# Performance work log

Measured on AMD Instinct MI355X. Metric: run time of the kernel, lower is better.

Reference implementation:

```python
import jax, jax.numpy as jnp
import numpy as np

IN_FEATURES = 4096
OUT_FEATURES = 11008
NUM_GROUPS = 4


def setup_inputs() -> dict:
    key = jax.random.key(0)
    k1, k2, k3 = jax.random.split(key, 3)
    inp = jax.random.normal(k1, (16, IN_FEATURES), dtype=jnp.float32)
    # packed int2 weights: each byte holds 4 ternary values (stored biased by +1 in 2 bits)
    weight_packed = jax.random.randint(k2, (OUT_FEATURES, IN_FEATURES // 4), 0, 256, dtype=jnp.int32)
    weight_scale = jax.random.uniform(k3, (NUM_GROUPS,), dtype=jnp.float32, minval=0.5, maxval=1.5)
    return {"input": inp, "weight_packed": weight_packed, "weight_scale": weight_scale}


def _unpack_int2(weight_packed):
    # [M, K/4] packed bytes -> [M, K] ternary values in {-1, 0, 1, 2}
    p = weight_packed
    M, Kp = p.shape
    w = jnp.stack([p & 3, (p >> 2) & 3, (p >> 4) & 3, (p >> 6) & 3], axis=-1)
    return w.reshape(M, Kp * 4).astype(jnp.float32) - 1.0


def reference(input, weight_packed, weight_scale):
    # per-row int8 activation quantization
    s = 127.0 / jnp.clip(jnp.max(jnp.abs(input), axis=-1, keepdims=True), 1e-5)  # [B,1]
    q = jnp.clip(jnp.round(input * s), -128.0, 127.0)  # int8-valued floats [B,K]
    w = _unpack_int2(weight_packed)  # [M,K]
    out = q @ w.T  # [B,M] integer-valued accumulation
    M = weight_packed.shape[0]
    rows_per_group = M // weight_scale.shape[0]
    col_scale = jnp.repeat(weight_scale, rows_per_group)  # [M] per-output-group scale
    return out * (1.0 / s) * col_scale
```

## Files before the change

### kernel.cpp

```cpp
#include <hip/hip_runtime.h>
#include <stdint.h>

#define K_DIM 4096
#define KW 1024
#define M_DIM 11008
#define B_DIM 16
#define GROUP_ROWS 2752
#define QTR_W 256

typedef int v4i __attribute__((ext_vector_type(4)));

__device__ __forceinline__ int spread2(int p) {
    int t = p | (p << 12);
    return (t & 0x00030003) | (((t >> 2) & 0x00030003) << 8);
}

__global__ __launch_bounds__(1024) void quant_k(const float* __restrict__ in,
                                                int* __restrict__ qg,
                                                int* __restrict__ sumq,
                                                float* __restrict__ invs) {
    const int b = blockIdx.x, t = threadIdx.x;
    const int lane = t & 63, wid = t >> 6;

    float4 v = ((const float4*)(in + (size_t)b * K_DIM))[t];
    float mx = fmaxf(fmaxf(fabsf(v.x), fabsf(v.y)), fmaxf(fabsf(v.z), fabsf(v.w)));
#pragma unroll
    for (int s = 1; s < 64; s <<= 1) mx = fmaxf(mx, __shfl_xor(mx, s, 64));

    __shared__ float wmax[16];
    __shared__ int wsum[16];
    if (lane == 0) wmax[wid] = mx;
    __syncthreads();
    float bm = wmax[0];
#pragma unroll
    for (int i = 1; i < 16; ++i) bm = fmaxf(bm, wmax[i]);
    const float sc = 127.f / fmaxf(bm, 1e-5f);

    float xs[4] = {v.x, v.y, v.z, v.w};
    int w = 0, ss = 0;
#pragma unroll
    for (int j = 0; j < 4; ++j) {
        int q = (int)rintf(xs[j] * sc);
        q = q > 127 ? 127 : (q < -128 ? -128 : q);
        ss += q;
        w |= (q & 255) << (8 * j);
    }
    qg[b * KW + t] = w;

#pragma unroll
    for (int s = 1; s < 64; s <<= 1) ss += __shfl_xor(ss, s, 64);
    if (lane == 0) wsum[wid] = ss;
    __syncthreads();
    if (t == 0) {
        int tot = 0;
#pragma unroll
        for (int i = 0; i < 16; ++i) tot += wsum[i];
        sumq[b] = tot;
        invs[b] = fmaxf(bm, 1e-5f) / 127.f;
    }
}

__global__ __launch_bounds__(256) void gemm_k(const int* __restrict__ wp,
                                              const int* __restrict__ qg,
                                              const int* __restrict__ sumq,
                                              const float* __restrict__ invs,
                                              const float* __restrict__ wscale,
                                              float* __restrict__ out) {
    __shared__ v4i buf[2][1024];
    const int t = threadIdx.x, lane = t & 63, wid = t >> 6;
    const int m0 = blockIdx.x * 16;
    const int lrow = lane & 15;
    const int lgrp = lane >> 4;

    const int* qbase = qg + lrow * KW + wid * 64 + lgrp * 4;

    v4i acc = {0, 0, 0, 0};
    v4i wst[4];
    v4i qb[2][4];

#pragma unroll
    for (int r = 0; r < 4; ++r) {
        const int row = r * 4 + wid;
        wst[r] = *(const v4i*)(wp + (size_t)(m0 + row) * KW + lane * 4);
    }
#pragma unroll
    for (int s = 0; s < 4; ++s) qb[0][s] = *(const v4i*)(qbase + s * 16);
#pragma unroll
    for (int r = 0; r < 4; ++r) {
        const int row = r * 4 + wid;
        buf[0][row * 64 + (lane ^ (row & 7))] = wst[r];
    }
    asm volatile("s_waitcnt lgkmcnt(0)" ::: "memory");
    asm volatile("s_barrier" ::: "memory");

#pragma unroll
    for (int q = 0; q < 4; ++q) {
        if (q < 3) {
#pragma unroll
            for (int r = 0; r < 4; ++r) {
                const int row = r * 4 + wid;
                wst[r] = *(const v4i*)(wp + (size_t)(m0 + row) * KW + (q + 1) * QTR_W + lane * 4);
            }
#pragma unroll
            for (int s = 0; s < 4; ++s)
                qb[(q + 1) & 1][s] = *(const v4i*)(qbase + (q + 1) * QTR_W + s * 16);
        }
#pragma unroll
        for (int s = 0; s < 4; ++s) {
            const int c = wid * 16 + s * 4 + lgrp;
            v4i wv = buf[q & 1][lrow * 64 + (c ^ (lrow & 7))];
            v4i bb;
            bb[0] = spread2(wv[0]); bb[1] = spread2(wv[1]);
            bb[2] = spread2(wv[2]); bb[3] = spread2(wv[3]);
            acc = __builtin_amdgcn_mfma_i32_16x16x64_i8(qb[q & 1][s], bb, acc, 0, 0, 0);
        }
        asm volatile("s_barrier" ::: "memory");
        if (q < 3) {
#pragma unroll
            for (int r = 0; r < 4; ++r) {
                const int row = r * 4 + wid;
                buf[(q + 1) & 1][row * 64 + (lane ^ (row & 7))] = wst[r];
            }
            asm volatile("s_waitcnt lgkmcnt(0)" ::: "memory");
            asm volatile("s_barrier" ::: "memory");
        }
    }

    buf[0][wid * 64 + lane] = acc;
    asm volatile("s_waitcnt lgkmcnt(0)" ::: "memory");
    asm volatile("s_barrier" ::: "memory");

    const int b = t >> 4, m = t & 15;
    const int src_lane = ((b >> 2) << 4) | m;
    const int reg = b & 3;
    const int* red = (const int*)&buf[0][0];
    int sum = red[(0 * 64 + src_lane) * 4 + reg] + red[(1 * 64 + src_lane) * 4 + reg] +
              red[(2 * 64 + src_lane) * 4 + reg] + red[(3 * 64 + src_lane) * 4 + reg];
    const float val = (float)(sum - sumq[b]) * invs[b] * wscale[m0 / GROUP_ROWS];
    out[(size_t)b * M_DIM + m0 + m] = val;
}

extern "C" void kernel_launch(void* const* d_in, const int* in_sizes, int n_in,
                              void* d_out, int out_size, void* d_ws, size_t ws_size,
                              hipStream_t stream) {
    const float* inp    = (const float*)d_in[0];
    const int*   wp     = (const int*)d_in[1];
    const float* wscale = (const float*)d_in[2];
    float* out = (float*)d_out;

    int*   qg   = (int*)d_ws;
    int*   sumq = qg + B_DIM * KW;
    float* invs = (float*)(sumq + B_DIM);

    quant_k<<<dim3(B_DIM), dim3(1024), 0, stream>>>(inp, qg, sumq, invs);
    gemm_k<<<dim3(M_DIM / 16), dim3(256), 0, stream>>>(wp, qg, sumq, invs, wscale, out);
}
```

Measured before the change: 21.24 us.

## Stream weights via direct global-to-LDS loads with triple buffering and split quant kernel

The GEMM kernel now loads packed weights straight into LDS with global_load_lds into a three-stage ring buffer, prefetching two quarters ahead and synchronising with vmcnt waits. This replaces the old register staging and extra LDS write barriers. All quantized activations are preloaded into registers up front. The quant kernel is split into 64 blocks of 256 threads, each redoing the row max, and writes partial sums that the GEMM adds up. The cost is more register pressure and redundant max computation.

Result: slower. 30.35 us (+42.9%).

```diff
diff --git a/kernel.cpp b/kernel.cpp
--- a/kernel.cpp
+++ b/kernel.cpp
@@ -15,28 +15,42 @@
     return (t & 0x00030003) | (((t >> 2) & 0x00030003) << 8);
 }
 
-__global__ __launch_bounds__(1024) void quant_k(const float* __restrict__ in,
-                                                int* __restrict__ qg,
-                                                int* __restrict__ sumq,
-                                                float* __restrict__ invs) {
-    const int b = blockIdx.x, t = threadIdx.x;
-    const int lane = t & 63, wid = t >> 6;
+__device__ __forceinline__ void gload_lds16(const int* g, int* l) {
+    __builtin_amdgcn_global_load_lds(
+        (const __attribute__((address_space(1))) unsigned int*)g,
+        (__attribute__((address_space(3))) unsigned int*)l, 16, 0, 0);
+}
 
-    float4 v = ((const float4*)(in + (size_t)b * K_DIM))[t];
-    float mx = fmaxf(fmaxf(fabsf(v.x), fabsf(v.y)), fmaxf(fabsf(v.z), fabsf(v.w)));
+__global__ __launch_bounds__(256) void quant_k(const float* __restrict__ in,
+                                               int* __restrict__ qg,
+                                               int* __restrict__ sumq_part,
+                                               float* __restrict__ invs) {
+    const int g = blockIdx.x, b = g >> 2, qt = g & 3;
+    const int t = threadIdx.x, lane = t & 63, wid = t >> 6;
+
+    const float4* row = (const float4*)(in + (size_t)b * K_DIM);
+    float4 v[4];
+#pragma unroll
+    for (int i = 0; i < 4; ++i) v[i] = row[t + i * 256];
+
+    float mx = 0.f;
+#pragma unroll
+    for (int i = 0; i < 4; ++i) {
+        mx = fmaxf(mx, fabsf(v[i].x)); mx = fmaxf(mx, fabsf(v[i].y));
+        mx = fmaxf(mx, fabsf(v[i].z)); mx = fmaxf(mx, fabsf(v[i].w));
+    }
 #pragma unroll
     for (int s = 1; s < 64; s <<= 1) mx = fmaxf(mx, __shfl_xor(mx, s, 64));
 
-    __shared__ float wmax[16];
-    __shared__ int wsum[16];
+    __shared__ float wmax[4];
+    __shared__ int wsum[4];
     if (lane == 0) wmax[wid] = mx;
     __syncthreads();
-    float bm = wmax[0];
-#pragma unroll
-    for (int i = 1; i < 16; ++i) bm = fmaxf(bm, wmax[i]);
+    const float bm = fmaxf(fmaxf(wmax[0], wmax[1]), fmaxf(wmax[2], wmax[3]));
     const float sc = 127.f / fmaxf(bm, 1e-5f);
 
-    float xs[4] = {v.x, v.y, v.z, v.w};
+    const float4 mine = v[qt];
+    float xs[4] = {mine.x, mine.y, mine.z, mine.w};
     int w = 0, ss = 0;
 #pragma unroll
     for (int j = 0; j < 4; ++j) {
@@ -45,98 +59,86 @@
         ss += q;
         w |= (q & 255) << (8 * j);
     }
-    qg[b * KW + t] = w;
+    qg[b * KW + qt * QTR_W + t] = w;
 
 #pragma unroll
     for (int s = 1; s < 64; s <<= 1) ss += __shfl_xor(ss, s, 64);
     if (lane == 0) wsum[wid] = ss;
     __syncthreads();
     if (t == 0) {
-        int tot = 0;
-#pragma unroll
-        for (int i = 0; i < 16; ++i) tot += wsum[i];
-        sumq[b] = tot;
-        invs[b] = fmaxf(bm, 1e-5f) / 127.f;
+        sumq_part[b * 4 + qt] = wsum[0] + wsum[1] + wsum[2] + wsum[3];
+        if (qt == 0) invs[b] = fmaxf(bm, 1e-5f) / 127.f;
     }
 }
 
-__global__ __launch_bounds__(256) void gemm_k(const int* __restrict__ wp,
-                                              const int* __restrict__ qg,
-                                              const int* __restrict__ sumq,
-                                              const float* __restrict__ invs,
-                                              const float* __restrict__ wscale,
-                                              float* __restrict__ out) {
-    __shared__ v4i buf[2][1024];
+__global__ __launch_bounds__(256, 4) void gemm_k(const int* __restrict__ wp,
+                                                 const int* __restrict__ qg,
+                                                 const int* __restrict__ sumq_part,
+                                                 const float* __restrict__ invs,
+                                                 const float* __restrict__ wscale,
+                                                 float* __restrict__ out) {
+    __shared__ v4i bufv[3 * 1024];
+    int* bufi = (int*)bufv;
     const int t = threadIdx.x, lane = t & 63, wid = t >> 6;
     const int m0 = blockIdx.x * 16;
     const int lrow = lane & 15;
     const int lgrp = lane >> 4;
 
-    const int* qbase = qg + lrow * KW + wid * 64 + lgrp * 4;
+    v4i qr[16];
+#pragma unroll
+    for (int i = 0; i < 16; ++i) {
+        const int qq = i >> 2, s = i & 3;
+        qr[i] = *(const v4i*)(qg + lrow * KW + qq * QTR_W + wid * 64 + s * 16 + lgrp * 4);
+    }
+#pragma unroll
+    for (int qq = 0; qq < 2; ++qq) {
+#pragma unroll
+        for (int r = 0; r < 4; ++r) {
+            const int row = r * 4 + wid;
+            gload_lds16(wp + (size_t)(m0 + row) * KW + qq * QTR_W + (lane ^ (row & 7)) * 4,
+                        bufi + qq * 4096 + row * 256);
+        }
+    }
 
     v4i acc = {0, 0, 0, 0};
-    v4i wst[4];
-    v4i qb[2][4];
-
-#pragma unroll
-    for (int r = 0; r < 4; ++r) {
-        const int row = r * 4 + wid;
-        wst[r] = *(const v4i*)(wp + (size_t)(m0 + row) * KW + lane * 4);
-    }
-#pragma unroll
-    for (int s = 0; s < 4; ++s) qb[0][s] = *(const v4i*)(qbase + s * 16);
-#pragma unroll
-    for (int r = 0; r < 4; ++r) {
-        const int row = r * 4 + wid;
-        buf[0][row * 64 + (lane ^ (row & 7))] = wst[r];
-    }
-    asm volatile("s_waitcnt lgkmcnt(0)" ::: "memory");
-    asm volatile("s_barrier" ::: "memory");
 
 #pragma unroll
     for (int q = 0; q < 4; ++q) {
-        if (q < 3) {
+        if (q < 3) asm volatile("s_waitcnt vmcnt(4)" ::: "memory");
+        else       asm volatile("s_waitcnt vmcnt(0)" ::: "memory");
+        asm volatile("s_barrier" ::: "memory");
+        if (q < 2) {
+            const int nb = (q + 2) % 3;
 #pragma unroll
             for (int r = 0; r < 4; ++r) {
                 const int row = r * 4 + wid;
-                wst[r] = *(const v4i*)(wp + (size_t)(m0 + row) * KW + (q + 1) * QTR_W + lane * 4);
+                gload_lds16(wp + (size_t)(m0 + row) * KW + (q + 2) * QTR_W + (lane ^ (row & 7)) * 4,
+                            bufi + nb * 4096 + row * 256);
             }
-#pragma unroll
-            for (int s = 0; s < 4; ++s)
-                qb[(q + 1) & 1][s] = *(const v4i*)(qbase + (q + 1) * QTR_W + s * 16);
         }
 #pragma unroll
         for (int s = 0; s < 4; ++s) {
             const int c = wid * 16 + s * 4 + lgrp;
-            v4i wv = buf[q & 1][lrow * 64 + (c ^ (lrow & 7))];
+            v4i wv = bufv[(q % 3) * 1024 + lrow * 64 + (c ^ (lrow & 7))];
             v4i bb;
             bb[0] = spread2(wv[0]); bb[1] = spread2(wv[1]);
             bb[2] = spread2(wv[2]); bb[3] = spread2(wv[3]);
-            acc = __builtin_amdgcn_mfma_i32_16x16x64_i8(qb[q & 1][s], bb, acc, 0, 0, 0);
-        }
-        asm volatile("s_barrier" ::: "memory");
-        if (q < 3) {
-#pragma unroll
-            for (int r = 0; r < 4; ++r) {
-                const int row = r * 4 + wid;
-                buf[(q + 1) & 1][row * 64 + (lane ^ (row & 7))] = wst[r];
-            }
-            asm volatile("s_waitcnt lgkmcnt(0)" ::: "memory");
-            asm volatile("s_barrier" ::: "memory");
+            acc = __builtin_amdgcn_mfma_i32_16x16x64_i8(qr[q * 4 + s], bb, acc, 0, 0, 0);
         }
     }
 
-    buf[0][wid * 64 + lane] = acc;
-    asm volatile("s_waitcnt lgkmcnt(0)" ::: "memory");
-    asm volatile("s_barrier" ::: "memory");
+    __syncthreads();
+    bufv[wid * 64 + lane] = acc;
+    __syncthreads();
 
     const int b = t >> 4, m = t & 15;
     const int src_lane = ((b >> 2) << 4) | m;
     const int reg = b & 3;
-    const int* red = (const int*)&buf[0][0];
-    int sum = red[(0 * 64 + src_lane) * 4 + reg] + red[(1 * 64 + src_lane) * 4 + reg] +
-              red[(2 * 64 + src_lane) * 4 + reg] + red[(3 * 64 + src_lane) * 4 + reg];
-    const float val = (float)(sum - sumq[b]) * invs[b] * wscale[m0 / GROUP_ROWS];
+    int sum = bufi[(0 * 64 + src_lane) * 4 + reg] + bufi[(1 * 64 + src_lane) * 4 + reg] +
+              bufi[(2 * 64 + src_lane) * 4 + reg] + bufi[(3 * 64 + src_lane) * 4 + reg];
+    const int sq = sumq_part[b * 4 + 0] + sumq_part[b * 4 + 1] +
+                   sumq_part[b * 4 + 2] + sumq_part[b * 4 + 3];
+    const float val = (float)(sum - sq) * invs[b] * wscale[m0 / GROUP_ROWS];
     out[(size_t)b * M_DIM + m0 + m] = val;
 }
 
@@ -149,9 +151,9 @@
     float* out = (float*)d_out;
 
     int*   qg   = (int*)d_ws;
-    int*   sumq = qg + B_DIM * KW;
-    float* invs = (float*)(sumq + B_DIM);
+    int*   sqp  = qg + B_DIM * KW;
+    float* invs = (float*)(sqp + B_DIM * 4);
 
-    quant_k<<<dim3(B_DIM), dim3(1024), 0, stream>>>(inp, qg, sumq, invs);
-    gemm_k<<<dim3(M_DIM / 16), dim3(256), 0, stream>>>(wp, qg, sumq, invs, wscale, out);
+    quant_k<<<dim3(B_DIM * 4), dim3(256), 0, stream>>>(inp, qg, sqp, invs);
+    gemm_k<<<dim3(M_DIM / 16), dim3(256), 0, stream>>>(wp, qg, sqp, invs, wscale, out);
 }
```

## Fuse activation quantization into a persistent GEMM kernel with register-held activations

Applied to the files above, without the earlier changes.

Merges the quantization kernel and the int2 GEMM into a single persistent kernel of 256 blocks that loop over 16-row weight tiles. Every block recomputes the int8 quantization of all 16 activation rows into LDS and keeps its slice in registers. Each iteration stages a full-K weight tile in LDS while prefetching the next tile into registers. This removes one launch and the global round trip for quantized activations, at the cost of redundant quantization work per block, a 64KB LDS footprint, and fewer blocks in flight.

Result: slower. 24.34 us (+14.6%).

```diff
diff --git a/kernel.cpp b/kernel.cpp
--- a/kernel.cpp
+++ b/kernel.cpp
@@ -6,138 +6,138 @@
 #define M_DIM 11008
 #define B_DIM 16
 #define GROUP_ROWS 2752
-#define QTR_W 256
+#define NTILES 688
+#define NBLK 256
+#define THREADS 512
 
-typedef int v4i __attribute__((ext_vector_type(4)));
+typedef int   v4i __attribute__((ext_vector_type(4)));
+typedef float v4f __attribute__((ext_vector_type(4)));
 
 __device__ __forceinline__ int spread2(int p) {
     int t = p | (p << 12);
     return (t & 0x00030003) | (((t >> 2) & 0x00030003) << 8);
 }
 
-__global__ __launch_bounds__(1024) void quant_k(const float* __restrict__ in,
-                                                int* __restrict__ qg,
-                                                int* __restrict__ sumq,
-                                                float* __restrict__ invs) {
-    const int b = blockIdx.x, t = threadIdx.x;
-    const int lane = t & 63, wid = t >> 6;
+__global__ __launch_bounds__(THREADS, 2) void fused_k(const float* __restrict__ in,
+                                                      const int* __restrict__ wp,
+                                                      const float* __restrict__ wscale,
+                                                      float* __restrict__ out) {
+    __shared__ int wlds[B_DIM * KW];
+    __shared__ int red[8 * 64 * 4];
+    __shared__ float sm_invs[B_DIM];
+    __shared__ int   sm_sumq[B_DIM];
+    __shared__ float sm_ws[4];
 
-    float4 v = ((const float4*)(in + (size_t)b * K_DIM))[t];
-    float mx = fmaxf(fmaxf(fabsf(v.x), fabsf(v.y)), fmaxf(fabsf(v.z), fabsf(v.w)));
+    const int t = threadIdx.x, lane = t & 63, wid = t >> 6;
+    const int lrow = lane & 15;
+    const int lgrp = (lane >> 4) & 3;
+    const int r = t >> 5, j = t & 31;
+    const int bid = blockIdx.x;
+
+    int tile = bid;
+    v4i wst[8];
+    {
+        const int* wb = wp + (size_t)(tile * 16 + r) * KW;
 #pragma unroll
-    for (int s = 1; s < 64; s <<= 1) mx = fmaxf(mx, __shfl_xor(mx, s, 64));
+        for (int i = 0; i < 8; ++i) wst[i] = *(const v4i*)(wb + (j + i * 32) * 4);
+    }
 
-    __shared__ float wmax[16];
-    __shared__ int wsum[16];
-    if (lane == 0) wmax[wid] = mx;
-    __syncthreads();
-    float bm = wmax[0];
+    const float* irow = in + (size_t)r * K_DIM;
+    float mx = 0.f;
 #pragma unroll
-    for (int i = 1; i < 16; ++i) bm = fmaxf(bm, wmax[i]);
-    const float sc = 127.f / fmaxf(bm, 1e-5f);
-
-    float xs[4] = {v.x, v.y, v.z, v.w};
-    int w = 0, ss = 0;
+    for (int i = 0; i < 8; ++i) {
+        const float* gp = irow + (j + i * 32) * 16;
 #pragma unroll
-    for (int j = 0; j < 4; ++j) {
-        int q = (int)rintf(xs[j] * sc);
-        q = q > 127 ? 127 : (q < -128 ? -128 : q);
-        ss += q;
-        w |= (q & 255) << (8 * j);
-    }
-    qg[b * KW + t] = w;
-
-#pragma unroll
-    for (int s = 1; s < 64; s <<= 1) ss += __shfl_xor(ss, s, 64);
-    if (lane == 0) wsum[wid] = ss;
-    __syncthreads();
-    if (t == 0) {
-        int tot = 0;
-#pragma unroll
-        for (int i = 0; i < 16; ++i) tot += wsum[i];
-        sumq[b] = tot;
-        invs[b] = fmaxf(bm, 1e-5f) / 127.f;
-    }
-}
-
-__global__ __launch_bounds__(256) void gemm_k(const int* __restrict__ wp,
-                                              const int* __restrict__ qg,
-                                              const int* __restrict__ sumq,
-                                              const float* __restrict__ invs,
-                                              const float* __restrict__ wscale,
-                                              float* __restrict__ out) {
-    __shared__ v4i buf[2][1024];
-    const int t = threadIdx.x, lane = t & 63, wid = t >> 6;
-    const int m0 = blockIdx.x * 16;
-    const int lrow = lane & 15;
-    const int lgrp = lane >> 4;
-
-    const int* qbase = qg + lrow * KW + wid * 64 + lgrp * 4;
-
-    v4i acc = {0, 0, 0, 0};
-    v4i wst[4];
-    v4i qb[2][4];
-
-#pragma unroll
-    for (int r = 0; r < 4; ++r) {
-        const int row = r * 4 + wid;
-        wst[r] = *(const v4i*)(wp + (size_t)(m0 + row) * KW + lane * 4);
+        for (int c = 0; c < 4; ++c) {
+            v4f v = *(const v4f*)(gp + c * 4);
+            mx = fmaxf(mx, fmaxf(fmaxf(fabsf(v[0]), fabsf(v[1])),
+                                 fmaxf(fabsf(v[2]), fabsf(v[3]))));
+        }
     }
 #pragma unroll
-    for (int s = 0; s < 4; ++s) qb[0][s] = *(const v4i*)(qbase + s * 16);
+    for (int s = 1; s < 32; s <<= 1) mx = fmaxf(mx, __shfl_xor(mx, s, 32));
+    const float bm = fmaxf(mx, 1e-5f);
+    const float sc = 127.f / bm;
+
+    int ss = 0;
 #pragma unroll
-    for (int r = 0; r < 4; ++r) {
-        const int row = r * 4 + wid;
-        buf[0][row * 64 + (lane ^ (row & 7))] = wst[r];
+    for (int i = 0; i < 8; ++i) {
+        const int g = j + i * 32;
+        const float* gp = irow + g * 16;
+        int w4[4];
+#pragma unroll
+        for (int c = 0; c < 4; ++c) {
+            v4f v = *(const v4f*)(gp + c * 4);
+            int w = 0;
+#pragma unroll
+            for (int e = 0; e < 4; ++e) {
+                int q = (int)rintf(v[e] * sc);
+                q = q > 127 ? 127 : (q < -128 ? -128 : q);
+                ss += q;
+                w |= (q & 255) << (8 * e);
+            }
+            w4[c] = w;
+        }
+        *(v4i*)(wlds + r * KW + ((g ^ (r & 7)) * 4)) = *(v4i*)w4;
+    }
+#pragma unroll
+    for (int s = 1; s < 32; s <<= 1) ss += __shfl_xor(ss, s, 32);
+    if (j == 0) { sm_sumq[r] = ss; sm_invs[r] = bm / 127.f; }
+    if (t < 4) sm_ws[t] = wscale[t];
+    asm volatile("s_waitcnt lgkmcnt(0)" ::: "memory");
+    __builtin_amdgcn_s_barrier();
+
+    v4i qr[8];
+#pragma unroll
+    for (int s = 0; s < 8; ++s) {
+        const int g = wid * 32 + s * 4 + lgrp;
+        qr[s] = *(const v4i*)(wlds + lrow * KW + ((g ^ (lrow & 7)) * 4));
     }
     asm volatile("s_waitcnt lgkmcnt(0)" ::: "memory");
-    asm volatile("s_barrier" ::: "memory");
+    __builtin_amdgcn_s_barrier();
 
+    for (;;) {
+        const int m0 = tile * 16;
 #pragma unroll
-    for (int q = 0; q < 4; ++q) {
-        if (q < 3) {
+        for (int i = 0; i < 8; ++i)
+            *(v4i*)(wlds + r * KW + (((j + i * 32) ^ (r & 7)) * 4)) = wst[i];
+        asm volatile("s_waitcnt lgkmcnt(0)" ::: "memory");
+        __builtin_amdgcn_s_barrier();
+
+        const int ntile = tile + NBLK;
+        if (ntile < NTILES) {
+            const int* wb = wp + (size_t)(ntile * 16 + r) * KW;
 #pragma unroll
-            for (int r = 0; r < 4; ++r) {
-                const int row = r * 4 + wid;
-                wst[r] = *(const v4i*)(wp + (size_t)(m0 + row) * KW + (q + 1) * QTR_W + lane * 4);
-            }
+            for (int i = 0; i < 8; ++i) wst[i] = *(const v4i*)(wb + (j + i * 32) * 4);
+        }
+
+        v4i acc = {0, 0, 0, 0};
 #pragma unroll
-            for (int s = 0; s < 4; ++s)
-                qb[(q + 1) & 1][s] = *(const v4i*)(qbase + (q + 1) * QTR_W + s * 16);
-        }
-#pragma unroll
-        for (int s = 0; s < 4; ++s) {
-            const int c = wid * 16 + s * 4 + lgrp;
-            v4i wv = buf[q & 1][lrow * 64 + (c ^ (lrow & 7))];
+        for (int s = 0; s < 8; ++s) {
+            const int g = wid * 32 + s * 4 + lgrp;
+            v4i wv = *(const v4i*)(wlds + lrow * KW + ((g ^ (lrow & 7)) * 4));
             v4i bb;
             bb[0] = spread2(wv[0]); bb[1] = spread2(wv[1]);
             bb[2] = spread2(wv[2]); bb[3] = spread2(wv[3]);
-            acc = __builtin_amdgcn_mfma_i32_16x16x64_i8(qb[q & 1][s], bb, acc, 0, 0, 0);
+            acc = __builtin_amdgcn_mfma_i32_16x16x64_i8(qr[s], bb, acc, 0, 0, 0);
         }
-        asm volatile("s_barrier" ::: "memory");
-        if (q < 3) {
+
+        *(v4i*)(red + (wid * 64 + lane) * 4) = acc;
+        asm volatile("s_waitcnt lgkmcnt(0)" ::: "memory");
+        __builtin_amdgcn_s_barrier();
+        if (t < 256) {
+            const int b = t >> 4, m = t & 15;
+            const int sl = ((b >> 2) << 4) | m;
+            const int rg = b & 3;
+            int sum = 0;
 #pragma unroll
-            for (int r = 0; r < 4; ++r) {
-                const int row = r * 4 + wid;
-                buf[(q + 1) & 1][row * 64 + (lane ^ (row & 7))] = wst[r];
-            }
-            asm volatile("s_waitcnt lgkmcnt(0)" ::: "memory");
-            asm volatile("s_barrier" ::: "memory");
+            for (int w8 = 0; w8 < 8; ++w8) sum += red[(w8 * 64 + sl) * 4 + rg];
+            const float val = (float)(sum - sm_sumq[b]) * sm_invs[b] * sm_ws[m0 / GROUP_ROWS];
+            out[(size_t)b * M_DIM + m0 + m] = val;
         }
+        if (ntile >= NTILES) break;
+        tile = ntile;
     }
-
-    buf[0][wid * 64 + lane] = acc;
-    asm volatile("s_waitcnt lgkmcnt(0)" ::: "memory");
-    asm volatile("s_barrier" ::: "memory");
-
-    const int b = t >> 4, m = t & 15;
-    const int src_lane = ((b >> 2) << 4) | m;
-    const int reg = b & 3;
-    const int* red = (const int*)&buf[0][0];
-    int sum = red[(0 * 64 + src_lane) * 4 + reg] + red[(1 * 64 + src_lane) * 4 + reg] +
-              red[(2 * 64 + src_lane) * 4 + reg] + red[(3 * 64 + src_lane) * 4 + reg];
-    const float val = (float)(sum - sumq[b]) * invs[b] * wscale[m0 / GROUP_ROWS];
-    out[(size_t)b * M_DIM + m0 + m] = val;
 }
 
 extern "C" void kernel_launch(void* const* d_in, const int* in_sizes, int n_in,
@@ -148,10 +148,5 @@
     const float* wscale = (const float*)d_in[2];
     float* out = (float*)d_out;
 
-    int*   qg   = (int*)d_ws;
-    int*   sumq = qg + B_DIM * KW;
-    float* invs = (float*)(sumq + B_DIM);
-
-    quant_k<<<dim3(B_DIM), dim3(1024), 0, stream>>>(inp, qg, sumq, invs);
-    gemm_k<<<dim3(M_DIM / 16), dim3(256), 0, stream>>>(wp, qg, sumq, invs, wscale, out);
+    fused_k<<<dim3(NBLK), dim3(THREADS), 0, stream>>>(inp, wp, wscale, out);
 }
```
